# Performance work log

Hardware: AMD Instinct MI355X
Metric: run time of the kernel (lower is better)

Reference implementation:

```python
import jax, jax.numpy as jnp
import numpy as np

N_NODE = 100000
D_IN = 256
HEADS = 4
D_HEAD = 64
N_EDGE = 1600000
NEG_SLOPE = 0.2


def setup_inputs() -> dict:
    key = jax.random.key(0)
    ks = jax.random.split(key, 7)
    x = jax.random.normal(ks[0], (1,), dtype=jnp.float32)  # unused by forward (module uses emb.weight)
    edge_index = jax.random.randint(ks[1], (2, N_EDGE), 0, N_NODE, dtype=jnp.int64)
    # xavier-normal-ish scales
    emb_weight = jax.random.normal(ks[2], (N_NODE, D_IN), dtype=jnp.float32) * np.sqrt(2.0 / (N_NODE + D_IN))
    w_scale = np.sqrt(2.0 / (D_IN + HEADS * D_HEAD))
    W_l = jax.random.normal(ks[3], (D_IN, HEADS * D_HEAD), dtype=jnp.float32) * w_scale
    W_r = jax.random.normal(ks[4], (D_IN, HEADS * D_HEAD), dtype=jnp.float32) * w_scale
    att = jax.random.normal(ks[5], (HEADS, D_HEAD), dtype=jnp.float32) * np.sqrt(2.0 / D_HEAD)
    bias = jnp.zeros((D_HEAD,), dtype=jnp.float32)
    return {"x": x, "edge_index": edge_index, "emb_weight": emb_weight,
            "W_l": W_l, "W_r": W_r, "att": att, "bias": bias}


def reference(x, edge_index, emb_weight, W_l, W_r, att, bias):
    N = emb_weight.shape[0]
    # add self loops (PyG GATv2Conv default add_self_loops=True)
    loops = jnp.arange(N, dtype=edge_index.dtype)
    src = jnp.concatenate([edge_index[0], loops])  # source j (messages flow j -> i)
    dst = jnp.concatenate([edge_index[1], loops])  # target i

    # linear transforms: [N, H, C]
    xl = (emb_weight @ W_l).reshape(N, HEADS, D_HEAD)
    xr = (emb_weight @ W_r).reshape(N, HEADS, D_HEAD)

    # GATv2 edge scores: a^T LeakyReLU(x_l[j] + x_r[i])  -> [E, H]
    e = jax.nn.leaky_relu(xl[src] + xr[dst], negative_slope=NEG_SLOPE)
    score = jnp.einsum('ehc,hc->eh', e, att)

    # segment softmax over incoming edges of each dst node
    smax = jax.ops.segment_max(score, dst, num_segments=N)  # [N, H]
    score = jnp.exp(score - smax[dst])
    denom = jax.ops.segment_sum(score, dst, num_segments=N)
    alpha = score / (denom[dst] + 1e-16)  # [E, H]

    # weighted aggregate of x_l[src]
    out = jax.ops.segment_sum(alpha[:, :, None] * xl[src], dst, num_segments=N)  # [N, H, C]
    out = out.mean(axis=1) + bias  # concat=False -> average heads, then bias

    out = jax.nn.elu(out)
    # stack single embedding then mean over dim 1 is identity
    return out
```

## Files before the change

kernel.cpp:

```cpp
#include <hip/hip_runtime.h>
#include <hip/hip_bf16.h>
#include <stdint.h>

#define D_IN 256
#define NEG 0.2f

typedef unsigned short bf16_t;
typedef __attribute__((ext_vector_type(8))) short bfrag;
typedef __attribute__((ext_vector_type(4))) float ffrag;

__device__ __forceinline__ bf16_t f2bf(float f) {
  unsigned int u = __float_as_uint(f);
  unsigned int r = u + 0x7FFFu + ((u >> 16) & 1u);
  return (bf16_t)(r >> 16);
}
__device__ __forceinline__ unsigned int pk2(float a, float b) {
  return (unsigned int)f2bf(a) | ((unsigned int)f2bf(b) << 16);
}
__device__ __forceinline__ void ld4bf(const bf16_t* p, float* f) {
  uint2 u = *(const uint2*)p;
  f[0] = __uint_as_float(u.x << 16);
  f[1] = __uint_as_float(u.x & 0xFFFF0000u);
  f[2] = __uint_as_float(u.y << 16);
  f[3] = __uint_as_float(u.y & 0xFFFF0000u);
}

__global__ void k_zero(int* __restrict__ a, int n) {
  int i = blockIdx.x * 256 + threadIdx.x;
  if (i < n) a[i] = 0;
}

__global__ void k_hist(const int* __restrict__ dst, int E, int* __restrict__ deg) {
  int e = blockIdx.x * 256 + threadIdx.x;
  if (e < E) atomicAdd(&deg[dst[e]], 1);
}

__global__ __launch_bounds__(256) void k_scanA(const int* __restrict__ deg,
                                               int* __restrict__ offs,
                                               int* __restrict__ bsum, int N) {
  __shared__ int sh[256];
  int t = threadIdx.x;
  int base = blockIdx.x * 1024 + t * 4;
  int v[4];
#pragma unroll
  for (int q = 0; q < 4; q++) v[q] = (base + q < N) ? deg[base + q] : 0;
  int ls = v[0] + v[1] + v[2] + v[3];
  sh[t] = ls;
  __syncthreads();
  for (int ofs = 1; ofs < 256; ofs <<= 1) {
    int x = (t >= ofs) ? sh[t - ofs] : 0;
    __syncthreads();
    sh[t] += x;
    __syncthreads();
  }
  int run = sh[t] - ls;
#pragma unroll
  for (int q = 0; q < 4; q++) {
    if (base + q < N) offs[base + q] = run;
    run += v[q];
  }
  if (t == 255) bsum[blockIdx.x] = sh[255];
}

__global__ __launch_bounds__(128) void k_scanB(int* __restrict__ bsum, int* __restrict__ offs,
                                               int nb, int E, int N) {
  __shared__ int sh[128];
  int t = threadIdx.x;
  int v = (t < nb) ? bsum[t] : 0;
  sh[t] = v;
  __syncthreads();
  for (int ofs = 1; ofs < 128; ofs <<= 1) {
    int x = (t >= ofs) ? sh[t - ofs] : 0;
    __syncthreads();
    sh[t] += x;
    __syncthreads();
  }
  if (t < nb) bsum[t] = sh[t] - v;
  if (t == 0) offs[N] = E;
}

__global__ __launch_bounds__(256) void k_scanC(int* __restrict__ offs, int* __restrict__ cursor,
                                               const int* __restrict__ bsum, int N) {
  int t = threadIdx.x;
  int base = blockIdx.x * 1024 + t * 4;
  int add = bsum[blockIdx.x];
#pragma unroll
  for (int q = 0; q < 4; q++) {
    int i = base + q;
    if (i < N) {
      int o = offs[i] + add;
      offs[i] = o;
      cursor[i] = o;
    }
  }
}

__global__ void k_scatter(const int* __restrict__ src, const int* __restrict__ dst, int E,
                          int* __restrict__ cursor, int* __restrict__ csr) {
  int e = blockIdx.x * 256 + threadIdx.x;
  if (e < E) {
    int pos = atomicAdd(&cursor[dst[e]], 1);
    csr[pos] = src[e];
  }
}

__global__ void k_wt(const float* __restrict__ Wl, const float* __restrict__ Wr,
                     bf16_t* __restrict__ Wt) {
  int gid = blockIdx.x * 256 + threadIdx.x;
  int w = gid >> 16;
  int c = (gid >> 8) & 255;
  int k = gid & 255;
  const float* W = w ? Wr : Wl;
  Wt[gid] = f2bf(W[k * 256 + c]);
}

__global__ __launch_bounds__(256) void k_gemm_mfma(const float* __restrict__ emb,
                                                   const bf16_t* __restrict__ Wt,
                                                   bf16_t* __restrict__ xl,
                                                   bf16_t* __restrict__ xr, int N) {
  __shared__ bf16_t As[128][40];
  __shared__ bf16_t Bs[128][40];

  const int tid = threadIdx.x;
  const int row0 = blockIdx.x * 128;
  const int nt = blockIdx.y;
  const bf16_t* Wp = Wt + (size_t)(nt >> 1) * 65536;
  bf16_t* dst = (nt < 2) ? xl : xr;
  const int c0 = (nt & 1) * 128;

  const int wave = tid >> 6, lane = tid & 63;
  const int m0w = (wave & 1) * 64, n0w = (wave >> 1) * 64;
  const int fr = lane & 15;
  const int aq = (lane >> 4) * 8;

  const int srow = tid >> 1, sseg = (tid & 1) * 16;
  const int grow = row0 + srow;
  const bool aok = grow < N;
  const float* ap = emb + (size_t)grow * 256 + sseg;
  const bf16_t* bp = Wp + (size_t)(c0 + srow) * 256 + sseg;

  ffrag acc[4][4];
#pragma unroll
  for (int mi = 0; mi < 4; mi++)
#pragma unroll
    for (int ni = 0; ni < 4; ni++) acc[mi][ni] = (ffrag)0.f;

  for (int k0 = 0; k0 < 256; k0 += 32) {
    float4 f0 = make_float4(0, 0, 0, 0), f1 = f0, f2 = f0, f3 = f0;
    if (aok) {
      f0 = *(const float4*)(ap + k0);
      f1 = *(const float4*)(ap + k0 + 4);
      f2 = *(const float4*)(ap + k0 + 8);
      f3 = *(const float4*)(ap + k0 + 12);
    }
    uint4 bv0 = *(const uint4*)(bp + k0);
    uint4 bv1 = *(const uint4*)(bp + k0 + 8);
    __syncthreads();
    uint4 p0, p1;
    p0.x = pk2(f0.x, f0.y); p0.y = pk2(f0.z, f0.w);
    p0.z = pk2(f1.x, f1.y); p0.w = pk2(f1.z, f1.w);
    p1.x = pk2(f2.x, f2.y); p1.y = pk2(f2.z, f2.w);
    p1.z = pk2(f3.x, f3.y); p1.w = pk2(f3.z, f3.w);
    *(uint4*)&As[srow][sseg] = p0;
    *(uint4*)&As[srow][sseg + 8] = p1;
    *(uint4*)&Bs[srow][sseg] = bv0;
    *(uint4*)&Bs[srow][sseg + 8] = bv1;
    __syncthreads();

    bfrag af[4], bf[4];
#pragma unroll
    for (int mi = 0; mi < 4; mi++) af[mi] = *(const bfrag*)&As[m0w + mi * 16 + fr][aq];
#pragma unroll
    for (int ni = 0; ni < 4; ni++) bf[ni] = *(const bfrag*)&Bs[n0w + ni * 16 + fr][aq];
#pragma unroll
    for (int mi = 0; mi < 4; mi++)
#pragma unroll
      for (int ni = 0; ni < 4; ni++)
        acc[mi][ni] = __builtin_amdgcn_mfma_f32_16x16x32_bf16(af[mi], bf[ni], acc[mi][ni], 0, 0, 0);
  }

  const int rbase = m0w + (lane >> 4) * 4;
#pragma unroll
  for (int mi = 0; mi < 4; mi++) {
#pragma unroll
    for (int ni = 0; ni < 4; ni++) {
      int col = c0 + n0w + ni * 16 + fr;
#pragma unroll
      for (int r = 0; r < 4; r++) {
        int row = row0 + rbase + mi * 16 + r;
        if (row < N) dst[(size_t)row * 256 + col] = f2bf(acc[mi][ni][r]);
      }
    }
  }
}

__device__ __forceinline__ float wred16(float p) {
  p += __shfl_xor(p, 1);
  p += __shfl_xor(p, 2);
  p += __shfl_xor(p, 4);
  p += __shfl_xor(p, 8);
  return p;
}

__global__ __launch_bounds__(256) void k_edge(const bf16_t* __restrict__ xl,
                                              const bf16_t* __restrict__ xr,
                                              const int* __restrict__ offs,
                                              const int* __restrict__ csr,
                                              const float* __restrict__ att,
                                              const float* __restrict__ bias,
                                              float* __restrict__ out, int N) {
  const int wv = threadIdx.x >> 6;
  const int lane = threadIdx.x & 63;
  const int i = blockIdx.x * 4 + wv;
  if (i >= N) return;
  const int cbase = (lane >> 4) * 64 + (lane & 15) * 4;

  const float4 avv = *(const float4*)(att + cbase);
  const float av[4] = {avv.x, avv.y, avv.z, avv.w};
  float xrv[4], xlv[4];
  ld4bf(xr + (size_t)i * 256 + cbase, xrv);
  ld4bf(xl + (size_t)i * 256 + cbase, xlv);

  float part = 0.f;
#pragma unroll
  for (int q = 0; q < 4; q++) {
    float t = xlv[q] + xrv[q];
    t = fmaxf(t, NEG * t);
    part = fmaf(av[q], t, part);
  }
  float m = wred16(part), d = 1.f;
  float acc[4] = {xlv[0], xlv[1], xlv[2], xlv[3]};

  int k = offs[i];
  const int kend = offs[i + 1];

  for (; k + 4 <= kend; k += 4) {
    int j0 = csr[k], j1 = csr[k + 1], j2 = csr[k + 2], j3 = csr[k + 3];
    float x0[4], x1[4], x2[4], x3[4];
    ld4bf(xl + (size_t)j0 * 256 + cbase, x0);
    ld4bf(xl + (size_t)j1 * 256 + cbase, x1);
    ld4bf(xl + (size_t)j2 * 256 + cbase, x2);
    ld4bf(xl + (size_t)j3 * 256 + cbase, x3);
    float p0 = 0.f, p1 = 0.f, p2 = 0.f, p3 = 0.f;
#pragma unroll
    for (int q = 0; q < 4; q++) {
      float t0 = x0[q] + xrv[q], t1 = x1[q] + xrv[q];
      float t2 = x2[q] + xrv[q], t3 = x3[q] + xrv[q];
      t0 = fmaxf(t0, NEG * t0); t1 = fmaxf(t1, NEG * t1);
      t2 = fmaxf(t2, NEG * t2); t3 = fmaxf(t3, NEG * t3);
      p0 = fmaf(av[q], t0, p0); p1 = fmaf(av[q], t1, p1);
      p2 = fmaf(av[q], t2, p2); p3 = fmaf(av[q], t3, p3);
    }
    float s0 = wred16(p0), s1 = wred16(p1), s2 = wred16(p2), s3 = wred16(p3);
    float nm = fmaxf(m, fmaxf(fmaxf(s0, s1), fmaxf(s2, s3)));
    float ea = __expf(m - nm);
    float e0 = __expf(s0 - nm), e1 = __expf(s1 - nm);
    float e2 = __expf(s2 - nm), e3 = __expf(s3 - nm);
    d = fmaf(d, ea, (e0 + e1) + (e2 + e3));
#pragma unroll
    for (int q = 0; q < 4; q++)
      acc[q] = fmaf(acc[q], ea,
                    fmaf(e0, x0[q], e1 * x1[q]) + fmaf(e2, x2[q], e3 * x3[q]));
    m = nm;
  }
  for (; k < kend; ++k) {
    int j = csr[k];
    ld4bf(xl + (size_t)j * 256 + cbase, xlv);
    float p = 0.f;
#pragma unroll
    for (int q = 0; q < 4; q++) {
      float t = xlv[q] + xrv[q];
      t = fmaxf(t, NEG * t);
      p = fmaf(av[q], t, p);
    }
    float s = wred16(p);
    float nm = fmaxf(m, s);
    float ea = __expf(m - nm);
    float eb = __expf(s - nm);
    d = fmaf(d, ea, eb);
#pragma unroll
    for (int q = 0; q < 4; q++) acc[q] = fmaf(acc[q], ea, eb * xlv[q]);
    m = nm;
  }

  float inv = 0.25f / d;
  float v[4];
#pragma unroll
  for (int q = 0; q < 4; q++) v[q] = acc[q] * inv;
#pragma unroll
  for (int q = 0; q < 4; q++) {
    v[q] += __shfl_xor(v[q], 16);
    v[q] += __shfl_xor(v[q], 32);
  }
  if ((lane >> 4) == 0) {
    const float4 bq = *(const float4*)(bias + (lane & 15) * 4);
    const float bb[4] = {bq.x, bq.y, bq.z, bq.w};
    float o[4];
#pragma unroll
    for (int q = 0; q < 4; q++) {
      float x = v[q] + bb[q];
      o[q] = x > 0.f ? x : (__expf(x) - 1.f);
    }
    *(float4*)(out + (size_t)i * 64 + (lane & 15) * 4) = make_float4(o[0], o[1], o[2], o[3]);
  }
}

extern "C" void kernel_launch(void* const* d_in, const int* in_sizes, int n_in,
                              void* d_out, int out_size, void* d_ws, size_t ws_size,
                              hipStream_t stream) {
  const int* edge = (const int*)d_in[1];
  const float* emb = (const float*)d_in[2];
  const float* Wl = (const float*)d_in[3];
  const float* Wr = (const float*)d_in[4];
  const float* att = (const float*)d_in[5];
  const float* bias = (const float*)d_in[6];
  float* out = (float*)d_out;

  const int E = in_sizes[1] / 2;
  const int N = in_sizes[2] / D_IN;
  const int* src = edge;
  const int* dst = edge + E;

  char* w = (char*)d_ws;
  bf16_t* xl = (bf16_t*)w;      w += (size_t)N * 256 * 2;
  bf16_t* xr = (bf16_t*)w;      w += (size_t)N * 256 * 2;
  bf16_t* Wt = (bf16_t*)w;      w += (size_t)2 * 256 * 256 * 2;
  int* offs = (int*)w;          w += ((size_t)N + 64) * 4;
  int* cursor = (int*)w;        w += ((size_t)N + 64) * 4;
  int* bsum = (int*)w;          w += 1024;
  int* csr = (int*)w;           w += (size_t)E * 4;

  const int nb = (N + 1023) / 1024;

  hipLaunchKernelGGL(k_zero, dim3((N + 255) / 256), dim3(256), 0, stream, cursor, N);
  hipLaunchKernelGGL(k_hist, dim3((E + 255) / 256), dim3(256), 0, stream, dst, E, cursor);
  hipLaunchKernelGGL(k_scanA, dim3(nb), dim3(256), 0, stream, cursor, offs, bsum, N);
  hipLaunchKernelGGL(k_scanB, dim3(1), dim3(128), 0, stream, bsum, offs, nb, E, N);
  hipLaunchKernelGGL(k_scanC, dim3(nb), dim3(256), 0, stream, offs, cursor, bsum, N);
  hipLaunchKernelGGL(k_scatter, dim3((E + 255) / 256), dim3(256), 0, stream, src, dst, E, cursor, csr);

  hipLaunchKernelGGL(k_wt, dim3(512), dim3(256), 0, stream, Wl, Wr, Wt);
  hipLaunchKernelGGL(k_gemm_mfma, dim3((N + 127) / 128, 4), dim3(256), 0, stream, emb, Wt, xl, xr, N);
  hipLaunchKernelGGL(k_edge, dim3((N + 3) / 4), dim3(256), 0, stream, xl, xr, offs, csr, att, bias, out, N);
}
```

Measured before the change: 558.7 us.

## Process four edges per wave with 16-lane heads and drop online softmax max

The edge kernel changes its lane mapping. Each 16-lane group now handles a different edge with 16 channels per lane, so a wave processes four neighbours at once with 128-bit loads. The running-max online softmax is replaced by plain exp accumulation without max subtraction, which is cheaper but risks overflow for large scores. Separately, the embedding is pre-converted to bf16 in its own pass so the GEMM reads half the bytes per tile. That conversion adds an extra full read and write of the embedding, and the path needs enough workspace.

```diff
diff --git a/kernel.cpp b/kernel.cpp
--- a/kernel.cpp
+++ b/kernel.cpp
@@ -17,12 +17,11 @@
 __device__ __forceinline__ unsigned int pk2(float a, float b) {
   return (unsigned int)f2bf(a) | ((unsigned int)f2bf(b) << 16);
 }
-__device__ __forceinline__ void ld4bf(const bf16_t* p, float* f) {
-  uint2 u = *(const uint2*)p;
-  f[0] = __uint_as_float(u.x << 16);
-  f[1] = __uint_as_float(u.x & 0xFFFF0000u);
-  f[2] = __uint_as_float(u.y << 16);
-  f[3] = __uint_as_float(u.y & 0xFFFF0000u);
+__device__ __forceinline__ void unpack8(uint4 u, float* f) {
+  f[0] = __uint_as_float(u.x << 16); f[1] = __uint_as_float(u.x & 0xFFFF0000u);
+  f[2] = __uint_as_float(u.y << 16); f[3] = __uint_as_float(u.y & 0xFFFF0000u);
+  f[4] = __uint_as_float(u.z << 16); f[5] = __uint_as_float(u.z & 0xFFFF0000u);
+  f[6] = __uint_as_float(u.w << 16); f[7] = __uint_as_float(u.w & 0xFFFF0000u);
 }
 
 __global__ void k_zero(int* __restrict__ a, int n) {
@@ -114,10 +113,94 @@
   Wt[gid] = f2bf(W[k * 256 + c]);
 }
 
-__global__ __launch_bounds__(256) void k_gemm_mfma(const float* __restrict__ emb,
-                                                   const bf16_t* __restrict__ Wt,
-                                                   bf16_t* __restrict__ xl,
-                                                   bf16_t* __restrict__ xr, int N) {
+__global__ void k_conv(const float* __restrict__ emb, bf16_t* __restrict__ embh, int n4) {
+  int i = blockIdx.x * 256 + threadIdx.x;
+  if (i < n4) {
+    float4 f = ((const float4*)emb)[i];
+    uint2 o;
+    o.x = pk2(f.x, f.y);
+    o.y = pk2(f.z, f.w);
+    ((uint2*)embh)[i] = o;
+  }
+}
+
+__global__ __launch_bounds__(256) void k_gemm_bf(const bf16_t* __restrict__ embh,
+                                                 const bf16_t* __restrict__ Wt,
+                                                 bf16_t* __restrict__ xl,
+                                                 bf16_t* __restrict__ xr, int N) {
+  __shared__ bf16_t As[128][40];
+  __shared__ bf16_t Bs[128][40];
+
+  const int tid = threadIdx.x;
+  const int row0 = blockIdx.x * 128;
+  const int nt = blockIdx.y;
+  const bf16_t* Wp = Wt + (size_t)(nt >> 1) * 65536;
+  bf16_t* dst = (nt < 2) ? xl : xr;
+  const int c0 = (nt & 1) * 128;
+
+  const int wave = tid >> 6, lane = tid & 63;
+  const int m0w = (wave & 1) * 64, n0w = (wave >> 1) * 64;
+  const int fr = lane & 15;
+  const int aq = (lane >> 4) * 8;
+
+  const int srow = tid >> 1, sseg = (tid & 1) * 16;
+  const int grow = row0 + srow;
+  const bool aok = grow < N;
+  const bf16_t* ap = embh + (size_t)grow * 256 + sseg;
+  const bf16_t* bp = Wp + (size_t)(c0 + srow) * 256 + sseg;
+
+  ffrag acc[4][4];
+#pragma unroll
+  for (int mi = 0; mi < 4; mi++)
+#pragma unroll
+    for (int ni = 0; ni < 4; ni++) acc[mi][ni] = (ffrag)0.f;
+
+  for (int k0 = 0; k0 < 256; k0 += 32) {
+    uint4 a0 = make_uint4(0, 0, 0, 0), a1 = a0;
+    if (aok) {
+      a0 = *(const uint4*)(ap + k0);
+      a1 = *(const uint4*)(ap + k0 + 8);
+    }
+    uint4 b0 = *(const uint4*)(bp + k0);
+    uint4 b1 = *(const uint4*)(bp + k0 + 8);
+    __syncthreads();
+    *(uint4*)&As[srow][sseg] = a0;
+    *(uint4*)&As[srow][sseg + 8] = a1;
+    *(uint4*)&Bs[srow][sseg] = b0;
+    *(uint4*)&Bs[srow][sseg + 8] = b1;
+    __syncthreads();
+
+    bfrag af[4], bfv[4];
+#pragma unroll
+    for (int mi = 0; mi < 4; mi++) af[mi] = *(const bfrag*)&As[m0w + mi * 16 + fr][aq];
+#pragma unroll
+    for (int ni = 0; ni < 4; ni++) bfv[ni] = *(const bfrag*)&Bs[n0w + ni * 16 + fr][aq];
+#pragma unroll
+    for (int mi = 0; mi < 4; mi++)
+#pragma unroll
+      for (int ni = 0; ni < 4; ni++)
+        acc[mi][ni] = __builtin_amdgcn_mfma_f32_16x16x32_bf16(af[mi], bfv[ni], acc[mi][ni], 0, 0, 0);
+  }
+
+  const int rbase = m0w + (lane >> 4) * 4;
+#pragma unroll
+  for (int mi = 0; mi < 4; mi++) {
+#pragma unroll
+    for (int ni = 0; ni < 4; ni++) {
+      int col = c0 + n0w + ni * 16 + fr;
+#pragma unroll
+      for (int r = 0; r < 4; r++) {
+        int row = row0 + rbase + mi * 16 + r;
+        if (row < N) dst[(size_t)row * 256 + col] = f2bf(acc[mi][ni][r]);
+      }
+    }
+  }
+}
+
+__global__ __launch_bounds__(256) void k_gemm_f32(const float* __restrict__ emb,
+                                                  const bf16_t* __restrict__ Wt,
+                                                  bf16_t* __restrict__ xl,
+                                                  bf16_t* __restrict__ xr, int N) {
   __shared__ bf16_t As[128][40];
   __shared__ bf16_t Bs[128][40];
 
@@ -153,8 +236,8 @@
       f2 = *(const float4*)(ap + k0 + 8);
       f3 = *(const float4*)(ap + k0 + 12);
     }
-    uint4 bv0 = *(const uint4*)(bp + k0);
-    uint4 bv1 = *(const uint4*)(bp + k0 + 8);
+    uint4 b0 = *(const uint4*)(bp + k0);
+    uint4 b1 = *(const uint4*)(bp + k0 + 8);
     __syncthreads();
     uint4 p0, p1;
     p0.x = pk2(f0.x, f0.y); p0.y = pk2(f0.z, f0.w);
@@ -163,20 +246,20 @@
     p1.z = pk2(f3.x, f3.y); p1.w = pk2(f3.z, f3.w);
     *(uint4*)&As[srow][sseg] = p0;
     *(uint4*)&As[srow][sseg + 8] = p1;
-    *(uint4*)&Bs[srow][sseg] = bv0;
-    *(uint4*)&Bs[srow][sseg + 8] = bv1;
-    __syncthreads();
-
-    bfrag af[4], bf[4];
+    *(uint4*)&Bs[srow][sseg] = b0;
+    *(uint4*)&Bs[srow][sseg + 8] = b1;
+    __syncthreads();
+
+    bfrag af[4], bfv[4];
 #pragma unroll
     for (int mi = 0; mi < 4; mi++) af[mi] = *(const bfrag*)&As[m0w + mi * 16 + fr][aq];
 #pragma unroll
-    for (int ni = 0; ni < 4; ni++) bf[ni] = *(const bfrag*)&Bs[n0w + ni * 16 + fr][aq];
+    for (int ni = 0; ni < 4; ni++) bfv[ni] = *(const bfrag*)&Bs[n0w + ni * 16 + fr][aq];
 #pragma unroll
     for (int mi = 0; mi < 4; mi++)
 #pragma unroll
       for (int ni = 0; ni < 4; ni++)
-        acc[mi][ni] = __builtin_amdgcn_mfma_f32_16x16x32_bf16(af[mi], bf[ni], acc[mi][ni], 0, 0, 0);
+        acc[mi][ni] = __builtin_amdgcn_mfma_f32_16x16x32_bf16(af[mi], bfv[ni], acc[mi][ni], 0, 0, 0);
   }
 
   const int rbase = m0w + (lane >> 4) * 4;
@@ -192,14 +275,6 @@
       }
     }
   }
-}
-
-__device__ __forceinline__ float wred16(float p) {
-  p += __shfl_xor(p, 1);
-  p += __shfl_xor(p, 2);
-  p += __shfl_xor(p, 4);
-  p += __shfl_xor(p, 8);
-  return p;
 }
 
 __global__ __launch_bounds__(256) void k_edge(const bf16_t* __restrict__ xl,
@@ -208,100 +283,97 @@
                                               const int* __restrict__ csr,
                                               const float* __restrict__ att,
                                               const float* __restrict__ bias,
-                                              float* __restrict__ out, int N) {
+                                              float* __restrict__ out, int N, int E) {
   const int wv = threadIdx.x >> 6;
   const int lane = threadIdx.x & 63;
   const int i = blockIdx.x * 4 + wv;
   if (i >= N) return;
-  const int cbase = (lane >> 4) * 64 + (lane & 15) * 4;
-
-  const float4 avv = *(const float4*)(att + cbase);
-  const float av[4] = {avv.x, avv.y, avv.z, avv.w};
-  float xrv[4], xlv[4];
-  ld4bf(xr + (size_t)i * 256 + cbase, xrv);
-  ld4bf(xl + (size_t)i * 256 + cbase, xlv);
-
-  float part = 0.f;
-#pragma unroll
-  for (int q = 0; q < 4; q++) {
-    float t = xlv[q] + xrv[q];
-    t = fmaxf(t, NEG * t);
-    part = fmaf(av[q], t, part);
-  }
-  float m = wred16(part), d = 1.f;
-  float acc[4] = {xlv[0], xlv[1], xlv[2], xlv[3]};
-
-  int k = offs[i];
-  const int kend = offs[i + 1];
-
-  for (; k + 4 <= kend; k += 4) {
-    int j0 = csr[k], j1 = csr[k + 1], j2 = csr[k + 2], j3 = csr[k + 3];
-    float x0[4], x1[4], x2[4], x3[4];
-    ld4bf(xl + (size_t)j0 * 256 + cbase, x0);
-    ld4bf(xl + (size_t)j1 * 256 + cbase, x1);
-    ld4bf(xl + (size_t)j2 * 256 + cbase, x2);
-    ld4bf(xl + (size_t)j3 * 256 + cbase, x3);
-    float p0 = 0.f, p1 = 0.f, p2 = 0.f, p3 = 0.f;
-#pragma unroll
-    for (int q = 0; q < 4; q++) {
-      float t0 = x0[q] + xrv[q], t1 = x1[q] + xrv[q];
-      float t2 = x2[q] + xrv[q], t3 = x3[q] + xrv[q];
-      t0 = fmaxf(t0, NEG * t0); t1 = fmaxf(t1, NEG * t1);
-      t2 = fmaxf(t2, NEG * t2); t3 = fmaxf(t3, NEG * t3);
-      p0 = fmaf(av[q], t0, p0); p1 = fmaf(av[q], t1, p1);
-      p2 = fmaf(av[q], t2, p2); p3 = fmaf(av[q], t3, p3);
-    }
-    float s0 = wred16(p0), s1 = wred16(p1), s2 = wred16(p2), s3 = wred16(p3);
-    float nm = fmaxf(m, fmaxf(fmaxf(s0, s1), fmaxf(s2, s3)));
-    float ea = __expf(m - nm);
-    float e0 = __expf(s0 - nm), e1 = __expf(s1 - nm);
-    float e2 = __expf(s2 - nm), e3 = __expf(s3 - nm);
-    d = fmaf(d, ea, (e0 + e1) + (e2 + e3));
-#pragma unroll
-    for (int q = 0; q < 4; q++)
-      acc[q] = fmaf(acc[q], ea,
-                    fmaf(e0, x0[q], e1 * x1[q]) + fmaf(e2, x2[q], e3 * x3[q]));
-    m = nm;
-  }
-  for (; k < kend; ++k) {
-    int j = csr[k];
-    ld4bf(xl + (size_t)j * 256 + cbase, xlv);
-    float p = 0.f;
-#pragma unroll
-    for (int q = 0; q < 4; q++) {
-      float t = xlv[q] + xrv[q];
+  const int g = lane >> 4, ls = lane & 15;
+  const int cb = ls * 16;
+
+  float attv[16], xrv[16];
+#pragma unroll
+  for (int q4 = 0; q4 < 4; q4++) {
+    float4 t = *(const float4*)(att + cb + q4 * 4);
+    attv[q4 * 4 + 0] = t.x; attv[q4 * 4 + 1] = t.y;
+    attv[q4 * 4 + 2] = t.z; attv[q4 * 4 + 3] = t.w;
+  }
+  {
+    const bf16_t* xp = xr + (size_t)i * 256 + cb;
+    unpack8(*(const uint4*)xp, xrv);
+    unpack8(*(const uint4*)(xp + 8), xrv + 8);
+  }
+
+  float acc[16];
+#pragma unroll
+  for (int q = 0; q < 16; q++) acc[q] = 0.f;
+  float d = 0.f;
+
+  const int kbeg = offs[i], kend = offs[i + 1];
+  const int nv = kend - kbeg + 1;
+
+  for (int p = 0; p < nv; p += 4) {
+    int v = p + g;
+    bool act = v < nv;
+    int idx = kbeg + v - 1;
+    idx = idx < kbeg ? kbeg : idx;
+    idx = idx >= E ? E - 1 : idx;
+    int j = (v == 0) ? i : csr[idx];
+
+    const bf16_t* xp = xl + (size_t)j * 256 + cb;
+    uint4 u0 = *(const uint4*)xp;
+    uint4 u1 = *(const uint4*)(xp + 8);
+    float xv[16];
+    unpack8(u0, xv);
+    unpack8(u1, xv + 8);
+
+    float part = 0.f;
+#pragma unroll
+    for (int q = 0; q < 16; q++) {
+      float t = xv[q] + xrv[q];
       t = fmaxf(t, NEG * t);
-      p = fmaf(av[q], t, p);
-    }
-    float s = wred16(p);
-    float nm = fmaxf(m, s);
-    float ea = __expf(m - nm);
-    float eb = __expf(s - nm);
-    d = fmaf(d, ea, eb);
-#pragma unroll
-    for (int q = 0; q < 4; q++) acc[q] = fmaf(acc[q], ea, eb * xlv[q]);
-    m = nm;
+      part = fmaf(attv[q], t, part);
+    }
+    part += __shfl_xor(part, 1);
+    part += __shfl_xor(part, 2);
+
+    float e = act ? __expf(part) : 0.f;
+    d += e;
+#pragma unroll
+    for (int q = 0; q < 16; q++) acc[q] = fmaf(e, xv[q], acc[q]);
+  }
+
+  d += __shfl_xor(d, 16);
+  d += __shfl_xor(d, 32);
+#pragma unroll
+  for (int q = 0; q < 16; q++) {
+    acc[q] += __shfl_xor(acc[q], 16);
+    acc[q] += __shfl_xor(acc[q], 32);
   }
 
   float inv = 0.25f / d;
-  float v[4];
-#pragma unroll
-  for (int q = 0; q < 4; q++) v[q] = acc[q] * inv;
-#pragma unroll
-  for (int q = 0; q < 4; q++) {
-    v[q] += __shfl_xor(v[q], 16);
-    v[q] += __shfl_xor(v[q], 32);
-  }
-  if ((lane >> 4) == 0) {
-    const float4 bq = *(const float4*)(bias + (lane & 15) * 4);
-    const float bb[4] = {bq.x, bq.y, bq.z, bq.w};
-    float o[4];
-#pragma unroll
-    for (int q = 0; q < 4; q++) {
-      float x = v[q] + bb[q];
-      o[q] = x > 0.f ? x : (__expf(x) - 1.f);
-    }
-    *(float4*)(out + (size_t)i * 64 + (lane & 15) * 4) = make_float4(o[0], o[1], o[2], o[3]);
+  float vv[16];
+#pragma unroll
+  for (int q = 0; q < 16; q++) vv[q] = acc[q] * inv;
+#pragma unroll
+  for (int q = 0; q < 16; q++) {
+    vv[q] += __shfl_xor(vv[q], 4);
+    vv[q] += __shfl_xor(vv[q], 8);
+  }
+
+  if (g == 0 && ls < 4) {
+    float* op = out + (size_t)i * 64 + ls * 16;
+#pragma unroll
+    for (int q4 = 0; q4 < 4; q4++) {
+      float4 b4 = *(const float4*)(bias + ls * 16 + q4 * 4);
+      float o[4];
+#pragma unroll
+      for (int q = 0; q < 4; q++) {
+        float x = vv[q4 * 4 + q] + ((const float*)&b4)[q];
+        o[q] = x > 0.f ? x : (__expf(x) - 1.f);
+      }
+      *(float4*)(op + q4 * 4) = make_float4(o[0], o[1], o[2], o[3]);
+    }
   }
 }
 
@@ -321,14 +393,18 @@
   const int* src = edge;
   const int* dst = edge + E;
 
+  const size_t NB = (size_t)N * 256 * 2;
   char* w = (char*)d_ws;
-  bf16_t* xl = (bf16_t*)w;      w += (size_t)N * 256 * 2;
-  bf16_t* xr = (bf16_t*)w;      w += (size_t)N * 256 * 2;
-  bf16_t* Wt = (bf16_t*)w;      w += (size_t)2 * 256 * 256 * 2;
-  int* offs = (int*)w;          w += ((size_t)N + 64) * 4;
-  int* cursor = (int*)w;        w += ((size_t)N + 64) * 4;
-  int* bsum = (int*)w;          w += 1024;
-  int* csr = (int*)w;           w += (size_t)E * 4;
+  bf16_t* xl = (bf16_t*)w;  w += NB;
+  bf16_t* xr = (bf16_t*)w;  w += NB;
+  bf16_t* Wt = (bf16_t*)w;  w += (size_t)2 * 256 * 256 * 2;
+  int* offs = (int*)w;      w += ((size_t)N + 64) * 4;
+  int* cursor = (int*)w;    w += ((size_t)N + 64) * 4;
+  int* bsum = (int*)w;      w += 1024;
+  int* csr = (int*)w;       w += (size_t)E * 4;
+  bf16_t* embh = (bf16_t*)w;
+  const size_t need_big = (size_t)(w - (char*)d_ws) + NB;
+  const bool big = ws_size >= need_big;
 
   const int nb = (N + 1023) / 1024;
 
@@ -340,6 +416,13 @@
   hipLaunchKernelGGL(k_scatter, dim3((E + 255) / 256), dim3(256), 0, stream, src, dst, E, cursor, csr);
 
   hipLaunchKernelGGL(k_wt, dim3(512), dim3(256), 0, stream, Wl, Wr, Wt);
-  hipLaunchKernelGGL(k_gemm_mfma, dim3((N + 127) / 128, 4), dim3(256), 0, stream, emb, Wt, xl, xr, N);
-  hipLaunchKernelGGL(k_edge, dim3((N + 3) / 4), dim3(256), 0, stream, xl, xr, offs, csr, att, bias, out, N);
-}
+  if (big) {
+    const int n4 = N * 64;
+    hipLaunchKernelGGL(k_conv, dim3((n4 + 255) / 256), dim3(256), 0, stream, emb, embh, n4);
+    hipLaunchKernelGGL(k_gemm_bf, dim3((N + 127) / 128, 4), dim3(256), 0, stream, embh, Wt, xl, xr, N);
+  } else {
+    hipLaunchKernelGGL(k_gemm_f32, dim3((N + 127) / 128, 4), dim3(256), 0, stream, emb, Wt, xl, xr, N);
+  }
+
+  hipLaunchKernelGGL(k_edge, dim3((N + 3) / 4), dim3(256), 0, stream, xl, xr, offs, csr, att, bias, out, N, E);
+}
```

Result: slower. 586.3 us (+4.9%).

## Fuse preprocessing kernels, use atomic ranks for CSR scatter, drop online-softmax max

Applied to the files above, without the earlier changes.

Merges the zero and weight-transpose kernels into one launch. The histogram atomics now record each edge's rank, so the CSR scatter needs no second atomic pass and can run inside the GEMM launch. The embedding is pre-converted to bf16 when the workspace allows, which halves the A-operand bytes the GEMM reads across its four column tiles. The edge kernel drops the running-max rescaling and exponentiates raw scores, removing extra exp and FMA work; this relies on the scores staying small enough not to overflow.

```diff
diff --git a/kernel.cpp b/kernel.cpp
--- a/kernel.cpp
+++ b/kernel.cpp
@@ -25,14 +25,43 @@
   f[3] = __uint_as_float(u.y & 0xFFFF0000u);
 }
 
-__global__ void k_zero(int* __restrict__ a, int n) {
-  int i = blockIdx.x * 256 + threadIdx.x;
-  if (i < n) a[i] = 0;
-}
-
-__global__ void k_hist(const int* __restrict__ dst, int E, int* __restrict__ deg) {
-  int e = blockIdx.x * 256 + threadIdx.x;
-  if (e < E) atomicAdd(&deg[dst[e]], 1);
+__global__ __launch_bounds__(256) void k_zero_wt(int* __restrict__ deg, int n, int zb,
+                                                 const float* __restrict__ Wl,
+                                                 const float* __restrict__ Wr,
+                                                 bf16_t* __restrict__ Wt) {
+  const int b = blockIdx.x, tid = threadIdx.x;
+  if (b < zb) {
+    int i = b * 256 + tid;
+    if (i < n) deg[i] = 0;
+  } else {
+    int gid = (b - zb) * 256 + tid;
+    int w = gid >> 16;
+    int c = (gid >> 8) & 255;
+    int k = gid & 255;
+    const float* W = w ? Wr : Wl;
+    Wt[gid] = f2bf(W[k * 256 + c]);
+  }
+}
+
+__global__ __launch_bounds__(256) void k_hist_conv(const int* __restrict__ dst, int E,
+                                                   int* __restrict__ deg, int* __restrict__ rank,
+                                                   int hb,
+                                                   const float* __restrict__ emb,
+                                                   bf16_t* __restrict__ embh, int n4) {
+  const int b = blockIdx.x, tid = threadIdx.x;
+  if (b < hb) {
+    int e = b * 256 + tid;
+    if (e < E) rank[e] = atomicAdd(&deg[dst[e]], 1);
+  } else {
+    int i = (b - hb) * 256 + tid;
+    if (i < n4) {
+      float4 f = ((const float4*)emb)[i];
+      uint2 o;
+      o.x = pk2(f.x, f.y);
+      o.y = pk2(f.z, f.w);
+      ((uint2*)embh)[i] = o;
+    }
+  }
 }
 
 __global__ __launch_bounds__(256) void k_scanA(const int* __restrict__ deg,
@@ -79,7 +108,7 @@
   if (t == 0) offs[N] = E;
 }
 
-__global__ __launch_bounds__(256) void k_scanC(int* __restrict__ offs, int* __restrict__ cursor,
+__global__ __launch_bounds__(256) void k_scanC(int* __restrict__ offs,
                                                const int* __restrict__ bsum, int N) {
   int t = threadIdx.x;
   int base = blockIdx.x * 1024 + t * 4;
@@ -87,45 +116,34 @@
 #pragma unroll
   for (int q = 0; q < 4; q++) {
     int i = base + q;
-    if (i < N) {
-      int o = offs[i] + add;
-      offs[i] = o;
-      cursor[i] = o;
-    }
-  }
-}
-
-__global__ void k_scatter(const int* __restrict__ src, const int* __restrict__ dst, int E,
-                          int* __restrict__ cursor, int* __restrict__ csr) {
-  int e = blockIdx.x * 256 + threadIdx.x;
-  if (e < E) {
-    int pos = atomicAdd(&cursor[dst[e]], 1);
-    csr[pos] = src[e];
-  }
-}
-
-__global__ void k_wt(const float* __restrict__ Wl, const float* __restrict__ Wr,
-                     bf16_t* __restrict__ Wt) {
-  int gid = blockIdx.x * 256 + threadIdx.x;
-  int w = gid >> 16;
-  int c = (gid >> 8) & 255;
-  int k = gid & 255;
-  const float* W = w ? Wr : Wl;
-  Wt[gid] = f2bf(W[k * 256 + c]);
-}
-
-__global__ __launch_bounds__(256) void k_gemm_mfma(const float* __restrict__ emb,
-                                                   const bf16_t* __restrict__ Wt,
-                                                   bf16_t* __restrict__ xl,
-                                                   bf16_t* __restrict__ xr, int N) {
+    if (i < N) offs[i] += add;
+  }
+}
+
+template <bool USEBF>
+__global__ __launch_bounds__(256) void k_gemm_scatter(
+    const float* __restrict__ emb, const bf16_t* __restrict__ embh,
+    const bf16_t* __restrict__ Wt, bf16_t* __restrict__ xl, bf16_t* __restrict__ xr,
+    const int* __restrict__ src, const int* __restrict__ dst,
+    const int* __restrict__ offs, const int* __restrict__ rank, int* __restrict__ csr,
+    int N, int E, int gb) {
   __shared__ bf16_t As[128][40];
   __shared__ bf16_t Bs[128][40];
-
   const int tid = threadIdx.x;
-  const int row0 = blockIdx.x * 128;
-  const int nt = blockIdx.y;
+
+  if ((int)blockIdx.x >= gb) {
+    int e = ((int)blockIdx.x - gb) * 256 + tid;
+    if (e < E) {
+      int pos = offs[dst[e]] + rank[e];
+      csr[pos] = src[e];
+    }
+    return;
+  }
+
+  const int bx = blockIdx.x >> 2, nt = blockIdx.x & 3;
+  const int row0 = bx * 128;
   const bf16_t* Wp = Wt + (size_t)(nt >> 1) * 65536;
-  bf16_t* dst = (nt < 2) ? xl : xr;
+  bf16_t* dstp = (nt < 2) ? xl : xr;
   const int c0 = (nt & 1) * 128;
 
   const int wave = tid >> 6, lane = tid & 63;
@@ -136,7 +154,6 @@
   const int srow = tid >> 1, sseg = (tid & 1) * 16;
   const int grow = row0 + srow;
   const bool aok = grow < N;
-  const float* ap = emb + (size_t)grow * 256 + sseg;
   const bf16_t* bp = Wp + (size_t)(c0 + srow) * 256 + sseg;
 
   ffrag acc[4][4];
@@ -146,37 +163,46 @@
     for (int ni = 0; ni < 4; ni++) acc[mi][ni] = (ffrag)0.f;
 
   for (int k0 = 0; k0 < 256; k0 += 32) {
-    float4 f0 = make_float4(0, 0, 0, 0), f1 = f0, f2 = f0, f3 = f0;
-    if (aok) {
-      f0 = *(const float4*)(ap + k0);
-      f1 = *(const float4*)(ap + k0 + 4);
-      f2 = *(const float4*)(ap + k0 + 8);
-      f3 = *(const float4*)(ap + k0 + 12);
-    }
-    uint4 bv0 = *(const uint4*)(bp + k0);
-    uint4 bv1 = *(const uint4*)(bp + k0 + 8);
-    __syncthreads();
-    uint4 p0, p1;
-    p0.x = pk2(f0.x, f0.y); p0.y = pk2(f0.z, f0.w);
-    p0.z = pk2(f1.x, f1.y); p0.w = pk2(f1.z, f1.w);
-    p1.x = pk2(f2.x, f2.y); p1.y = pk2(f2.z, f2.w);
-    p1.z = pk2(f3.x, f3.y); p1.w = pk2(f3.z, f3.w);
-    *(uint4*)&As[srow][sseg] = p0;
-    *(uint4*)&As[srow][sseg + 8] = p1;
-    *(uint4*)&Bs[srow][sseg] = bv0;
-    *(uint4*)&Bs[srow][sseg + 8] = bv1;
-    __syncthreads();
-
-    bfrag af[4], bf[4];
+    uint4 pa0 = make_uint4(0, 0, 0, 0), pa1 = pa0;
+    if (USEBF) {
+      const bf16_t* ap = embh + (size_t)grow * 256 + sseg;
+      if (aok) {
+        pa0 = *(const uint4*)(ap + k0);
+        pa1 = *(const uint4*)(ap + k0 + 8);
+      }
+    } else {
+      const float* ap = emb + (size_t)grow * 256 + sseg;
+      float4 f0 = make_float4(0, 0, 0, 0), f1 = f0, f2 = f0, f3 = f0;
+      if (aok) {
+        f0 = *(const float4*)(ap + k0);
+        f1 = *(const float4*)(ap + k0 + 4);
+        f2 = *(const float4*)(ap + k0 + 8);
+        f3 = *(const float4*)(ap + k0 + 12);
+      }
+      pa0.x = pk2(f0.x, f0.y); pa0.y = pk2(f0.z, f0.w);
+      pa0.z = pk2(f1.x, f1.y); pa0.w = pk2(f1.z, f1.w);
+      pa1.x = pk2(f2.x, f2.y); pa1.y = pk2(f2.z, f2.w);
+      pa1.z = pk2(f3.x, f3.y); pa1.w = pk2(f3.z, f3.w);
+    }
+    uint4 b0 = *(const uint4*)(bp + k0);
+    uint4 b1 = *(const uint4*)(bp + k0 + 8);
+    __syncthreads();
+    *(uint4*)&As[srow][sseg] = pa0;
+    *(uint4*)&As[srow][sseg + 8] = pa1;
+    *(uint4*)&Bs[srow][sseg] = b0;
+    *(uint4*)&Bs[srow][sseg + 8] = b1;
+    __syncthreads();
+
+    bfrag af[4], bfv[4];
 #pragma unroll
     for (int mi = 0; mi < 4; mi++) af[mi] = *(const bfrag*)&As[m0w + mi * 16 + fr][aq];
 #pragma unroll
-    for (int ni = 0; ni < 4; ni++) bf[ni] = *(const bfrag*)&Bs[n0w + ni * 16 + fr][aq];
+    for (int ni = 0; ni < 4; ni++) bfv[ni] = *(const bfrag*)&Bs[n0w + ni * 16 + fr][aq];
 #pragma unroll
     for (int mi = 0; mi < 4; mi++)
 #pragma unroll
       for (int ni = 0; ni < 4; ni++)
-        acc[mi][ni] = __builtin_amdgcn_mfma_f32_16x16x32_bf16(af[mi], bf[ni], acc[mi][ni], 0, 0, 0);
+        acc[mi][ni] = __builtin_amdgcn_mfma_f32_16x16x32_bf16(af[mi], bfv[ni], acc[mi][ni], 0, 0, 0);
   }
 
   const int rbase = m0w + (lane >> 4) * 4;
@@ -188,7 +214,7 @@
 #pragma unroll
       for (int r = 0; r < 4; r++) {
         int row = row0 + rbase + mi * 16 + r;
-        if (row < N) dst[(size_t)row * 256 + col] = f2bf(acc[mi][ni][r]);
+        if (row < N) dstp[(size_t)row * 256 + col] = f2bf(acc[mi][ni][r]);
       }
     }
   }
@@ -199,6 +225,16 @@
   p += __shfl_xor(p, 2);
   p += __shfl_xor(p, 4);
   p += __shfl_xor(p, 8);
+  return p;
+}
+__device__ __forceinline__ float dotleaky(const float* x, const float* xr, const float* av) {
+  float p = 0.f;
+#pragma unroll
+  for (int q = 0; q < 4; q++) {
+    float t = x[q] + xr[q];
+    t = fmaxf(t, NEG * t);
+    p = fmaf(av[q], t, p);
+  }
   return p;
 }
 
@@ -221,15 +257,10 @@
   ld4bf(xr + (size_t)i * 256 + cbase, xrv);
   ld4bf(xl + (size_t)i * 256 + cbase, xlv);
 
-  float part = 0.f;
-#pragma unroll
-  for (int q = 0; q < 4; q++) {
-    float t = xlv[q] + xrv[q];
-    t = fmaxf(t, NEG * t);
-    part = fmaf(av[q], t, part);
-  }
-  float m = wred16(part), d = 1.f;
-  float acc[4] = {xlv[0], xlv[1], xlv[2], xlv[3]};
+  float s = wred16(dotleaky(xlv, xrv, av));
+  float e = __expf(s);
+  float d = e;
+  float acc[4] = {e * xlv[0], e * xlv[1], e * xlv[2], e * xlv[3]};
 
   int k = offs[i];
   const int kend = offs[i + 1];
@@ -251,36 +282,20 @@
       p0 = fmaf(av[q], t0, p0); p1 = fmaf(av[q], t1, p1);
       p2 = fmaf(av[q], t2, p2); p3 = fmaf(av[q], t3, p3);
     }
-    float s0 = wred16(p0), s1 = wred16(p1), s2 = wred16(p2), s3 = wred16(p3);
-    float nm = fmaxf(m, fmaxf(fmaxf(s0, s1), fmaxf(s2, s3)));
-    float ea = __expf(m - nm);
-    float e0 = __expf(s0 - nm), e1 = __expf(s1 - nm);
-    float e2 = __expf(s2 - nm), e3 = __expf(s3 - nm);
-    d = fmaf(d, ea, (e0 + e1) + (e2 + e3));
+    float e0 = __expf(wred16(p0)), e1 = __expf(wred16(p1));
+    float e2 = __expf(wred16(p2)), e3 = __expf(wred16(p3));
+    d += (e0 + e1) + (e2 + e3);
 #pragma unroll
     for (int q = 0; q < 4; q++)
-      acc[q] = fmaf(acc[q], ea,
-                    fmaf(e0, x0[q], e1 * x1[q]) + fmaf(e2, x2[q], e3 * x3[q]));
-    m = nm;
+      acc[q] += fmaf(e0, x0[q], e1 * x1[q]) + fmaf(e2, x2[q], e3 * x3[q]);
   }
   for (; k < kend; ++k) {
     int j = csr[k];
     ld4bf(xl + (size_t)j * 256 + cbase, xlv);
-    float p = 0.f;
-#pragma unroll
-    for (int q = 0; q < 4; q++) {
-      float t = xlv[q] + xrv[q];
-      t = fmaxf(t, NEG * t);
-      p = fmaf(av[q], t, p);
-    }
-    float s = wred16(p);
-    float nm = fmaxf(m, s);
-    float ea = __expf(m - nm);
-    float eb = __expf(s - nm);
-    d = fmaf(d, ea, eb);
-#pragma unroll
-    for (int q = 0; q < 4; q++) acc[q] = fmaf(acc[q], ea, eb * xlv[q]);
-    m = nm;
+    float ee = __expf(wred16(dotleaky(xlv, xrv, av)));
+    d += ee;
+#pragma unroll
+    for (int q = 0; q < 4; q++) acc[q] = fmaf(ee, xlv[q], acc[q]);
   }
 
   float inv = 0.25f / d;
@@ -321,25 +336,41 @@
   const int* src = edge;
   const int* dst = edge + E;
 
+  const size_t NB = (size_t)N * 256 * 2;
   char* w = (char*)d_ws;
-  bf16_t* xl = (bf16_t*)w;      w += (size_t)N * 256 * 2;
-  bf16_t* xr = (bf16_t*)w;      w += (size_t)N * 256 * 2;
-  bf16_t* Wt = (bf16_t*)w;      w += (size_t)2 * 256 * 256 * 2;
-  int* offs = (int*)w;          w += ((size_t)N + 64) * 4;
-  int* cursor = (int*)w;        w += ((size_t)N + 64) * 4;
-  int* bsum = (int*)w;          w += 1024;
-  int* csr = (int*)w;           w += (size_t)E * 4;
+  bf16_t* xl = (bf16_t*)w;  w += NB;
+  bf16_t* xr = (bf16_t*)w;  w += NB;
+  bf16_t* Wt = (bf16_t*)w;  w += (size_t)2 * 256 * 256 * 2;
+  int* offs = (int*)w;      w += ((size_t)N + 64) * 4;
+  int* deg = (int*)w;       w += ((size_t)N + 64) * 4;
+  int* bsum = (int*)w;      w += 1024;
+  int* rank = (int*)w;      w += (size_t)E * 4;
+  int* csr = (int*)w;       w += (size_t)E * 4;
+  bf16_t* embh = (bf16_t*)w;
+  const size_t need_big = (size_t)(w - (char*)d_ws) + NB;
+  const bool big = ws_size >= need_big;
 
   const int nb = (N + 1023) / 1024;
-
-  hipLaunchKernelGGL(k_zero, dim3((N + 255) / 256), dim3(256), 0, stream, cursor, N);
-  hipLaunchKernelGGL(k_hist, dim3((E + 255) / 256), dim3(256), 0, stream, dst, E, cursor);
-  hipLaunchKernelGGL(k_scanA, dim3(nb), dim3(256), 0, stream, cursor, offs, bsum, N);
+  const int zb = (N + 255) / 256;
+  const int hb = (E + 255) / 256;
+  const int n4 = big ? N * 64 : 0;
+  const int cb = big ? (n4 + 255) / 256 : 0;
+  const int gb = ((N + 127) / 128) * 4;
+  const int sb = hb;
+
+  hipLaunchKernelGGL(k_zero_wt, dim3(zb + 512), dim3(256), 0, stream, deg, N, zb, Wl, Wr, Wt);
+  hipLaunchKernelGGL(k_hist_conv, dim3(hb + cb), dim3(256), 0, stream, dst, E, deg, rank, hb,
+                     emb, embh, n4);
+  hipLaunchKernelGGL(k_scanA, dim3(nb), dim3(256), 0, stream, deg, offs, bsum, N);
   hipLaunchKernelGGL(k_scanB, dim3(1), dim3(128), 0, stream, bsum, offs, nb, E, N);
-  hipLaunchKernelGGL(k_scanC, dim3(nb), dim3(256), 0, stream, offs, cursor, bsum, N);
-  hipLaunchKernelGGL(k_scatter, dim3((E + 255) / 256), dim3(256), 0, stream, src, dst, E, cursor, csr);
-
-  hipLaunchKernelGGL(k_wt, dim3(512), dim3(256), 0, stream, Wl, Wr, Wt);
-  hipLaunchKernelGGL(k_gemm_mfma, dim3((N + 127) / 128, 4), dim3(256), 0, stream, emb, Wt, xl, xr, N);
-  hipLaunchKernelGGL(k_edge, dim3((N + 3) / 4), dim3(256), 0, stream, xl, xr, offs, csr, att, bias, out, N);
-}
+  hipLaunchKernelGGL(k_scanC, dim3(nb), dim3(256), 0, stream, offs, bsum, N);
+  if (big) {
+    hipLaunchKernelGGL(k_gemm_scatter<true>, dim3(gb + sb), dim3(256), 0, stream,
+                       emb, embh, Wt, xl, xr, src, dst, offs, rank, csr, N, E, gb);
+  } else {
+    hipLaunchKernelGGL(k_gemm_scatter<false>, dim3(gb + sb), dim3(256), 0, stream,
+                       emb, embh, Wt, xl, xr, src, dst, offs, rank, csr, N, E, gb);
+  }
+  hipLaunchKernelGGL(k_edge, dim3((N + 3) / 4), dim3(256), 0, stream, xl, xr, offs, csr,
+                     att, bias, out, N);
+}
```

New measurement: 464.6 us. 1.2x faster.
